# Kernel tuning notes

Measured on AMD Instinct MI355X. Metric: run time of the kernel, lower is better.

The kernel has to match this reference:

```python
import jax, jax.numpy as jnp
import numpy as np

N_NODES = 100000
N_EDGES = 3200000
NFEAT, HID, NCLASS = 256, 32, 16


def setup_inputs() -> dict:
    key = jax.random.key(0)
    ks = jax.random.split(key, 6)
    x = jax.random.normal(ks[0], (N_NODES, NFEAT), dtype=jnp.float32)
    edge_index = jax.random.randint(ks[1], (2, N_EDGES), 0, N_NODES, dtype=jnp.int64)
    edge_weight = jax.random.uniform(ks[2], (N_EDGES,), dtype=jnp.float32)
    # Glorot-ish init for the two GCNConv linear weights; bias zeros (PyG default init zeros bias)
    W1 = jax.random.normal(ks[3], (NFEAT, HID), dtype=jnp.float32) * (1.0 / np.sqrt(NFEAT))
    b1 = jnp.zeros((HID,), dtype=jnp.float32)
    W2 = jax.random.normal(ks[4], (HID, NCLASS), dtype=jnp.float32) * (1.0 / np.sqrt(HID))
    b2 = jnp.zeros((NCLASS,), dtype=jnp.float32)
    return {"x": x, "edge_index": edge_index, "edge_weight": edge_weight,
            "W1": W1, "b1": b1, "W2": W2, "b2": b2}


def _gcn_norm(row, col, w, n):
    """PyG gcn_norm: add self-loops (weight 1), symmetric normalization."""
    loop = jnp.arange(n, dtype=row.dtype)
    row = jnp.concatenate([row, loop])
    col = jnp.concatenate([col, loop])
    w = jnp.concatenate([w, jnp.ones((n,), dtype=w.dtype)])
    deg = jax.ops.segment_sum(w, col, num_segments=n)  # degree at target nodes
    dinv = jnp.where(deg > 0, jax.lax.rsqrt(deg), 0.0)
    norm = dinv[row] * w * dinv[col]
    return row, col, norm


def _gcn_conv(x, W, b, row, col, norm, n):
    xw = x @ W                                  # [N, out]
    msg = xw[row] * norm[:, None]               # gather at source + scale
    out = jax.ops.segment_sum(msg, col, num_segments=n)  # scatter-add at target
    return out + b


def reference(x, edge_index, edge_weight, W1, b1, W2, b2):
    n = x.shape[0]
    row, col, norm = _gcn_norm(edge_index[0], edge_index[1], edge_weight, n)
    h = jax.nn.relu(_gcn_conv(x, W1, b1, row, col, norm, n))
    # dropout is identity in eval mode
    logits = _gcn_conv(h, W2, b2, row, col, norm, n)
    return jax.nn.log_softmax(logits, axis=1)
```

## Files before the change

### kernel.cpp

```cpp
#include <hip/hip_runtime.h>

#define N_NODES 100000
#define N_EDGES 3200000
#define NFEAT 256
#define HID 32
#define NCLASS 16

#define NB 32
#define CHUNK (N_EDGES / NB)
#define RN2 32768
#define NR2 ((N_NODES + RN2 - 1) / RN2)

#define SCAN_TPB 256
#define SCAN_EPB 1024
#define SCAN_NBLK ((N_NODES + SCAN_EPB - 1) / SCAN_EPB)

#define XPAD 261

__device__ inline unsigned short f2bf(float f) {
    unsigned u = __float_as_uint(f);
    u += 0x7FFFu + ((u >> 16) & 1u);
    return (unsigned short)(u >> 16);
}
__device__ inline float bf2f(unsigned short s) {
    return __uint_as_float((unsigned)s << 16);
}

__global__ __launch_bounds__(1024) void k_count(const int* __restrict__ col,
                                                unsigned* __restrict__ H) {
    __shared__ unsigned hist[RN2 / 2];
    int t = threadIdx.x, b = blockIdx.x, r = blockIdx.y;
    int base = r * RN2;
    const int* cc = col + (size_t)b * CHUNK;
    for (int i = t; i < RN2 / 2; i += 1024) hist[i] = 0;
    __syncthreads();
    for (int i = t; i < CHUNK; i += 1024) {
        unsigned d = (unsigned)cc[i] - (unsigned)base;
        if (d < RN2) atomicAdd(&hist[d >> 1], 1u << ((d & 1) * 16));
    }
    __syncthreads();
    int lim = min(RN2, N_NODES - base);
    unsigned* Hb = H + (size_t)b * N_NODES;
    for (int i = t; i < lim; i += 1024)
        Hb[base + i] = (hist[i >> 1] >> ((i & 1) * 16)) & 0xFFFFu;
}

__global__ void k_rowsum(const unsigned* __restrict__ H, int* __restrict__ cnt) {
    int n = blockIdx.x * 256 + threadIdx.x;
    if (n >= N_NODES) return;
    unsigned s = 0;
    #pragma unroll 8
    for (int b = 0; b < NB; ++b) s += H[(size_t)b * N_NODES + n];
    cnt[n] = (int)s;
}

__global__ __launch_bounds__(SCAN_TPB) void k_scanA(const int* __restrict__ cnt,
                                                    int* __restrict__ offs,
                                                    int* __restrict__ bsum) {
    __shared__ int s[SCAN_TPB];
    int t = threadIdx.x;
    int base = blockIdx.x * SCAN_EPB + t * 4;
    int v0 = (base + 0 < N_NODES) ? cnt[base + 0] : 0;
    int v1 = (base + 1 < N_NODES) ? cnt[base + 1] : 0;
    int v2 = (base + 2 < N_NODES) ? cnt[base + 2] : 0;
    int v3 = (base + 3 < N_NODES) ? cnt[base + 3] : 0;
    int sum = v0 + v1 + v2 + v3;
    s[t] = sum;
    __syncthreads();
    for (int off = 1; off < SCAN_TPB; off <<= 1) {
        int x = (t >= off) ? s[t - off] : 0;
        __syncthreads();
        s[t] += x;
        __syncthreads();
    }
    int excl = s[t] - sum;
    if (t == SCAN_TPB - 1) bsum[blockIdx.x] = s[t];
    int run = excl;
    if (base + 0 < N_NODES) offs[base + 0] = run; run += v0;
    if (base + 1 < N_NODES) offs[base + 1] = run; run += v1;
    if (base + 2 < N_NODES) offs[base + 2] = run; run += v2;
    if (base + 3 < N_NODES) offs[base + 3] = run;
}

__global__ __launch_bounds__(128) void k_scanB(int* __restrict__ bsum) {
    __shared__ int s[128];
    int t = threadIdx.x;
    int v = (t < SCAN_NBLK) ? bsum[t] : 0;
    s[t] = v;
    __syncthreads();
    for (int off = 1; off < 128; off <<= 1) {
        int x = (t >= off) ? s[t - off] : 0;
        __syncthreads();
        s[t] += x;
        __syncthreads();
    }
    if (t < SCAN_NBLK) bsum[t] = s[t] - v;
}

__global__ __launch_bounds__(SCAN_TPB) void k_scanC(int* __restrict__ offs,
                                                    const int* __restrict__ bsum) {
    int t = threadIdx.x;
    int add = bsum[blockIdx.x];
    int base = blockIdx.x * SCAN_EPB + t * 4;
    #pragma unroll
    for (int i = 0; i < 4; ++i) {
        int idx = base + i;
        if (idx < N_NODES) offs[idx] += add;
    }
    if (blockIdx.x == 0 && t == 0) offs[N_NODES] = N_EDGES;
}

__global__ void k_bprefix(unsigned* __restrict__ H, const int* __restrict__ offs) {
    int n = blockIdx.x * 256 + threadIdx.x;
    if (n >= N_NODES) return;
    unsigned run = (unsigned)offs[n];
    for (int b = 0; b < NB; ++b) {
        size_t idx = (size_t)b * N_NODES + n;
        unsigned v = H[idx];
        H[idx] = run;
        run += v;
    }
}

__global__ __launch_bounds__(1024) void k_place(const int* __restrict__ col,
                                                const unsigned* __restrict__ B,
                                                unsigned* __restrict__ perm) {
    __shared__ unsigned rk[RN2 / 2];
    int t = threadIdx.x, b = blockIdx.x, r = blockIdx.y;
    int base = r * RN2;
    size_t eb = (size_t)b * CHUNK;
    const unsigned* Bb = B + (size_t)b * N_NODES;
    for (int i = t; i < RN2 / 2; i += 1024) rk[i] = 0;
    __syncthreads();
    for (int i = t; i < CHUNK; i += 1024) {
        int c = col[eb + i];
        unsigned d = (unsigned)c - (unsigned)base;
        if (d < RN2) {
            unsigned old = atomicAdd(&rk[d >> 1], 1u << ((d & 1) * 16));
            unsigned rr = (old >> ((d & 1) * 16)) & 0xFFFFu;
            perm[eb + i] = Bb[c] + rr;
        }
    }
}

__global__ void k_emit(const int* __restrict__ row, const float* __restrict__ w,
                       const unsigned* __restrict__ perm, float2* __restrict__ ein) {
    int e = blockIdx.x * 256 + threadIdx.x;
    if (e < N_EDGES) ein[perm[e]] = make_float2(__int_as_float(row[e]), w[e]);
}

__global__ void k_deg(const float2* __restrict__ ein, const int* __restrict__ offs,
                      float* __restrict__ dinv) {
    int idx = blockIdx.x * 256 + threadIdx.x;
    int n = idx >> 2, l = idx & 3;
    if (n >= N_NODES) return;
    int s = offs[n], e = offs[n + 1];
    float sum = 0.f;
    for (int p = s + l; p < e; p += 4) sum += ein[p].y;
    sum += __shfl_xor(sum, 1, 4);
    sum += __shfl_xor(sum, 2, 4);
    if (l == 0) dinv[n] = rsqrtf(1.0f + sum);
}

__global__ void k_norm(float2* __restrict__ ein, const int* __restrict__ offs,
                       const float* __restrict__ dinv) {
    int idx = blockIdx.x * 256 + threadIdx.x;
    int n = idx >> 2, l = idx & 3;
    if (n >= N_NODES) return;
    float dn = dinv[n];
    int s = offs[n], e = offs[n + 1];
    for (int p = s + l; p < e; p += 4) {
        float2 v = ein[p];
        int src = __float_as_int(v.x);
        ein[p].y = dn * dinv[src] * v.y;
    }
}

__global__ __launch_bounds__(256) void k_gemm1s(const float* __restrict__ x,
                                                const float* __restrict__ W1,
                                                unsigned short* __restrict__ xwp) {
    __shared__ float sWc[16 * HID];
    __shared__ float sX[16 * XPAD];
    int t = threadIdx.x;
    long rowbase = (long)blockIdx.x * 256;
    int kbase = blockIdx.y * 64;
    unsigned short* xw = xwp + (size_t)blockIdx.y * N_NODES * HID;
    int tr = t >> 3;
    int tc = t & 7;
    float acc[8][4] = {};
    for (int k0 = kbase; k0 < kbase + 64; k0 += 16) {
        if (t < 128) *(float4*)&sWc[t * 4] = *(const float4*)&W1[k0 * HID + t * 4];
        #pragma unroll
        for (int p = 0; p < 4; ++p) {
            int rt = (t >> 2) + p * 64;
            int kk = (t & 3) * 4;
            long grow = rowbase + rt;
            float4 v = make_float4(0.f, 0.f, 0.f, 0.f);
            if (grow < N_NODES) v = *(const float4*)&x[grow * NFEAT + k0 + kk];
            sX[(kk + 0) * XPAD + rt] = v.x; sX[(kk + 1) * XPAD + rt] = v.y;
            sX[(kk + 2) * XPAD + rt] = v.z; sX[(kk + 3) * XPAD + rt] = v.w;
        }
        __syncthreads();
        #pragma unroll
        for (int kk = 0; kk < 16; ++kk) {
            float xv[8], wv[4];
            *(float4*)&xv[0] = *(float4*)&sX[kk * XPAD + tr * 8];
            *(float4*)&xv[4] = *(float4*)&sX[kk * XPAD + tr * 8 + 4];
            *(float4*)&wv[0] = *(float4*)&sWc[kk * HID + tc * 4];
            #pragma unroll
            for (int m = 0; m < 8; ++m)
                #pragma unroll
                for (int n = 0; n < 4; ++n)
                    acc[m][n] = fmaf(xv[m], wv[n], acc[m][n]);
        }
        __syncthreads();
    }
    #pragma unroll
    for (int m = 0; m < 8; ++m) {
        long r = rowbase + tr * 8 + m;
        if (r < N_NODES) {
            ushort4 o;
            o.x = f2bf(acc[m][0]); o.y = f2bf(acc[m][1]);
            o.z = f2bf(acc[m][2]); o.w = f2bf(acc[m][3]);
            *(ushort4*)&xw[r * HID + tc * 4] = o;
        }
    }
}

__global__ void k_comb(const unsigned short* __restrict__ xwp,
                       ushort4* __restrict__ xwb) {
    int i = blockIdx.x * 256 + threadIdx.x;
    const ushort4* p0 = (const ushort4*)xwp;
    const ushort4* p1 = p0 + 800000;
    const ushort4* p2 = p1 + 800000;
    const ushort4* p3 = p2 + 800000;
    ushort4 a = p0[i], b = p1[i], c = p2[i], d = p3[i];
    ushort4 o;
    o.x = f2bf(bf2f(a.x) + bf2f(b.x) + bf2f(c.x) + bf2f(d.x));
    o.y = f2bf(bf2f(a.y) + bf2f(b.y) + bf2f(c.y) + bf2f(d.y));
    o.z = f2bf(bf2f(a.z) + bf2f(b.z) + bf2f(c.z) + bf2f(d.z));
    o.w = f2bf(bf2f(a.w) + bf2f(b.w) + bf2f(c.w) + bf2f(d.w));
    xwb[i] = o;
}

__global__ __launch_bounds__(256) void k_gather1(const unsigned short* __restrict__ xwb,
                                                 const float* __restrict__ dinv,
                                                 const float2* __restrict__ ein,
                                                 const int* __restrict__ offs,
                                                 const float* __restrict__ b1,
                                                 float* __restrict__ h) {
    int idx = blockIdx.x * 256 + threadIdx.x;
    int n = idx >> 3, l = idx & 7;
    int c4 = l * 4;
    const ushort4* xb = (const ushort4*)xwb;
    float di = dinv[n];
    float dd = di * di;
    ushort4 q = xb[(long)n * 8 + l];
    float4 acc = make_float4(bf2f(q.x) * dd, bf2f(q.y) * dd,
                             bf2f(q.z) * dd, bf2f(q.w) * dd);
    int s = offs[n], e = offs[n + 1];
    for (int p0 = s; p0 < e; p0 += 8) {
        int pl = p0 + l;
        float2 pr = (pl < e) ? ein[pl] : make_float2(__int_as_float(n), 0.f);
        int ri = __float_as_int(pr.x);
        #pragma unroll
        for (int j = 0; j < 8; ++j) {
            int r = __shfl(ri, j, 8);
            float nm = __shfl(pr.y, j, 8);
            ushort4 g = xb[(long)r * 8 + l];
            acc.x = fmaf(bf2f(g.x), nm, acc.x);
            acc.y = fmaf(bf2f(g.y), nm, acc.y);
            acc.z = fmaf(bf2f(g.z), nm, acc.z);
            acc.w = fmaf(bf2f(g.w), nm, acc.w);
        }
    }
    float4 bb = *(const float4*)&b1[c4];
    acc.x = fmaxf(acc.x + bb.x, 0.f);
    acc.y = fmaxf(acc.y + bb.y, 0.f);
    acc.z = fmaxf(acc.z + bb.z, 0.f);
    acc.w = fmaxf(acc.w + bb.w, 0.f);
    *(float4*)&h[(long)n * HID + c4] = acc;
}

__global__ __launch_bounds__(256) void k_gemm2(const float* __restrict__ h,
                                               const float* __restrict__ W2,
                                               unsigned short* __restrict__ hwb) {
    __shared__ float sH[64][33];
    __shared__ float sW2[HID * NCLASS];
    int t = threadIdx.x;
    if (t < 128) {
        int idx = t * 4;
        *(float4*)&sW2[idx] = *(const float4*)&W2[idx];
    }
    long base = (long)blockIdx.x * 64;
    #pragma unroll
    for (int i = 0; i < 2; ++i) {
        int idx = t + i * 256;
        int rt = idx >> 3, kk = (idx & 7) * 4;
        long gr = base + rt;
        float4 v = make_float4(0.f, 0.f, 0.f, 0.f);
        if (gr < N_NODES) v = *(const float4*)&h[gr * HID + kk];
        sH[rt][kk + 0] = v.x; sH[rt][kk + 1] = v.y;
        sH[rt][kk + 2] = v.z; sH[rt][kk + 3] = v.w;
    }
    __syncthreads();
    int r = t >> 2, c4 = (t & 3) * 4;
    float acc[4] = {};
    #pragma unroll
    for (int k = 0; k < HID; ++k) {
        float hv = sH[r][k];
        float wv[4];
        *(float4*)&wv[0] = *(float4*)&sW2[k * NCLASS + c4];
        #pragma unroll
        for (int n = 0; n < 4; ++n) acc[n] = fmaf(hv, wv[n], acc[n]);
    }
    long gr = base + r;
    if (gr < N_NODES) {
        ushort4 o;
        o.x = f2bf(acc[0]); o.y = f2bf(acc[1]);
        o.z = f2bf(acc[2]); o.w = f2bf(acc[3]);
        *(ushort4*)&hwb[gr * NCLASS + c4] = o;
    }
}

__global__ __launch_bounds__(256) void k_gather2(const unsigned short* __restrict__ hwb,
                                                 const float* __restrict__ dinv,
                                                 const float2* __restrict__ ein,
                                                 const int* __restrict__ offs,
                                                 const float* __restrict__ b2,
                                                 float* __restrict__ out) {
    int idx = blockIdx.x * 256 + threadIdx.x;
    int n = idx >> 2, l = idx & 3;
    if (n >= N_NODES) return;
    int c4 = l * 4;
    const ushort4* hb = (const ushort4*)hwb;
    float di = dinv[n];
    float dd = di * di;
    ushort4 q = hb[(long)n * 4 + l];
    float4 acc = make_float4(bf2f(q.x) * dd, bf2f(q.y) * dd,
                             bf2f(q.z) * dd, bf2f(q.w) * dd);
    int s = offs[n], e = offs[n + 1];
    for (int p0 = s; p0 < e; p0 += 8) {
        int pl0 = p0 + l, pl1 = p0 + 4 + l;
        float2 pr0 = (pl0 < e) ? ein[pl0] : make_float2(__int_as_float(n), 0.f);
        float2 pr1 = (pl1 < e) ? ein[pl1] : make_float2(__int_as_float(n), 0.f);
        int r0 = __float_as_int(pr0.x), r1 = __float_as_int(pr1.x);
        #pragma unroll
        for (int j = 0; j < 4; ++j) {
            int r = __shfl(r0, j, 4);
            float nm = __shfl(pr0.y, j, 4);
            ushort4 g = hb[(long)r * 4 + l];
            acc.x = fmaf(bf2f(g.x), nm, acc.x);
            acc.y = fmaf(bf2f(g.y), nm, acc.y);
            acc.z = fmaf(bf2f(g.z), nm, acc.z);
            acc.w = fmaf(bf2f(g.w), nm, acc.w);
        }
        #pragma unroll
        for (int j = 0; j < 4; ++j) {
            int r = __shfl(r1, j, 4);
            float nm = __shfl(pr1.y, j, 4);
            ushort4 g = hb[(long)r * 4 + l];
            acc.x = fmaf(bf2f(g.x), nm, acc.x);
            acc.y = fmaf(bf2f(g.y), nm, acc.y);
            acc.z = fmaf(bf2f(g.z), nm, acc.z);
            acc.w = fmaf(bf2f(g.w), nm, acc.w);
        }
    }
    float4 bb = *(const float4*)&b2[c4];
    float vx = acc.x + bb.x, vy = acc.y + bb.y, vz = acc.z + bb.z, vw = acc.w + bb.w;
    float m = fmaxf(fmaxf(vx, vy), fmaxf(vz, vw));
    m = fmaxf(m, __shfl_xor(m, 1, 4));
    m = fmaxf(m, __shfl_xor(m, 2, 4));
    float sum = __expf(vx - m) + __expf(vy - m) + __expf(vz - m) + __expf(vw - m);
    sum += __shfl_xor(sum, 1, 4);
    sum += __shfl_xor(sum, 2, 4);
    float ls = m + __logf(sum);
    float4 o = make_float4(vx - ls, vy - ls, vz - ls, vw - ls);
    *(float4*)&out[(long)n * NCLASS + c4] = o;
}

extern "C" void kernel_launch(void* const* d_in, const int* in_sizes, int n_in,
                              void* d_out, int out_size, void* d_ws, size_t ws_size,
                              hipStream_t stream) {
    const float* x  = (const float*)d_in[0];
    const int*   ei = (const int*)d_in[1];
    const float* w  = (const float*)d_in[2];
    const float* W1 = (const float*)d_in[3];
    const float* b1 = (const float*)d_in[4];
    const float* W2 = (const float*)d_in[5];
    const float* b2 = (const float*)d_in[6];
    float* out = (float*)d_out;

    const int* row = ei;
    const int* col = ei + N_EDGES;

    float* ws = (float*)d_ws;
    float2* ein = (float2*)ws;
    unsigned* H = (unsigned*)(ws + 2 * (size_t)N_EDGES);
    unsigned* perm = (unsigned*)(ws + 2 * (size_t)N_EDGES + (size_t)NB * N_NODES);
    float* h = (float*)perm;
    float* dinv = ws + 2 * (size_t)N_EDGES + (size_t)NB * N_NODES + N_EDGES;
    int* cnt = (int*)(dinv + N_NODES);
    int* offs = cnt + N_NODES;
    int* bsum = offs + N_NODES + 1;
    size_t xwp_off = (size_t)(2 * (size_t)N_EDGES + (size_t)NB * N_NODES + N_EDGES
                              + 3 * N_NODES + 1 + 128);
    xwp_off = (xwp_off + 3) & ~(size_t)3;
    unsigned short* xwp = (unsigned short*)(ws + xwp_off);
    unsigned short* xwb = (unsigned short*)(ws + xwp_off + 6400000);
    unsigned short* hwb = xwb + (size_t)N_NODES * HID;

    const int B = 256;

    k_count<<<dim3(NB, NR2), 1024, 0, stream>>>(col, H);
    k_rowsum<<<(N_NODES + B - 1) / B, B, 0, stream>>>(H, cnt);
    k_scanA<<<SCAN_NBLK, SCAN_TPB, 0, stream>>>(cnt, offs, bsum);
    k_scanB<<<1, 128, 0, stream>>>(bsum);
    k_scanC<<<SCAN_NBLK, SCAN_TPB, 0, stream>>>(offs, bsum);
    k_bprefix<<<(N_NODES + B - 1) / B, B, 0, stream>>>(H, offs);
    k_place<<<dim3(NB, NR2), 1024, 0, stream>>>(col, H, perm);
    k_emit<<<(N_EDGES + B - 1) / B, B, 0, stream>>>(row, w, perm, ein);

    k_deg<<<(N_NODES * 4 + B - 1) / B, B, 0, stream>>>(ein, offs, dinv);
    k_norm<<<(N_NODES * 4 + B - 1) / B, B, 0, stream>>>(ein, offs, dinv);

    k_gemm1s<<<dim3((N_NODES + 255) / 256, 4), 256, 0, stream>>>(x, W1, xwp);
    k_comb<<<(N_NODES * HID / 4) / B, B, 0, stream>>>(xwp, (ushort4*)xwb);
    k_gather1<<<(N_NODES * 8) / B, B, 0, stream>>>(xwb, dinv, ein, offs, b1, h);

    k_gemm2<<<(N_NODES + 63) / 64, B, 0, stream>>>(h, W2, hwb);
    k_gather2<<<(N_NODES * 4 + B - 1) / B, B, 0, stream>>>(hwb, dinv, ein, offs, b2, out);
}
```

Measured before the change: 312.2 us.

## Fold edge normalization into gathers and retile first GEMM split-K

Removes the separate k_norm pass that rewrote every edge weight with dinv[src]*dinv[dst]. Instead the gathers scale each edge weight by dinv[src] at load time and apply the destination dinv once at the end. This avoids a full read-modify-write sweep over the 3.2M-edge array, at the price of an extra random dinv lookup per edge in both gathers. Separately, the first GEMM now uses 128-row tiles with 2-way split-K over 128 features instead of 256-row tiles with 4-way split-K. That halves the partial-result traffic that k_comb has to combine, but gives each thread less register blocking.

```diff
diff --git a/kernel.cpp b/kernel.cpp
--- a/kernel.cpp
+++ b/kernel.cpp
@@ -15,7 +15,7 @@
 #define SCAN_EPB 1024
 #define SCAN_NBLK ((N_NODES + SCAN_EPB - 1) / SCAN_EPB)
 
-#define XPAD 261
+#define XPAD 133
 
 __device__ inline unsigned short f2bf(float f) {
     unsigned u = __float_as_uint(f);
@@ -162,38 +162,24 @@
     if (l == 0) dinv[n] = rsqrtf(1.0f + sum);
 }
 
-__global__ void k_norm(float2* __restrict__ ein, const int* __restrict__ offs,
-                       const float* __restrict__ dinv) {
-    int idx = blockIdx.x * 256 + threadIdx.x;
-    int n = idx >> 2, l = idx & 3;
-    if (n >= N_NODES) return;
-    float dn = dinv[n];
-    int s = offs[n], e = offs[n + 1];
-    for (int p = s + l; p < e; p += 4) {
-        float2 v = ein[p];
-        int src = __float_as_int(v.x);
-        ein[p].y = dn * dinv[src] * v.y;
-    }
-}
-
 __global__ __launch_bounds__(256) void k_gemm1s(const float* __restrict__ x,
                                                 const float* __restrict__ W1,
                                                 unsigned short* __restrict__ xwp) {
-    __shared__ float sWc[16 * HID];
-    __shared__ float sX[16 * XPAD];
+    __shared__ float sWc[32 * HID];
+    __shared__ float sX[32 * XPAD];
     int t = threadIdx.x;
-    long rowbase = (long)blockIdx.x * 256;
-    int kbase = blockIdx.y * 64;
+    long rowbase = (long)blockIdx.x * 128;
+    int kbase = blockIdx.y * 128;
     unsigned short* xw = xwp + (size_t)blockIdx.y * N_NODES * HID;
     int tr = t >> 3;
     int tc = t & 7;
-    float acc[8][4] = {};
-    for (int k0 = kbase; k0 < kbase + 64; k0 += 16) {
-        if (t < 128) *(float4*)&sWc[t * 4] = *(const float4*)&W1[k0 * HID + t * 4];
+    float acc[4][4] = {};
+    for (int k0 = kbase; k0 < kbase + 128; k0 += 32) {
+        *(float4*)&sWc[t * 4] = *(const float4*)&W1[k0 * HID + t * 4];
         #pragma unroll
         for (int p = 0; p < 4; ++p) {
-            int rt = (t >> 2) + p * 64;
-            int kk = (t & 3) * 4;
+            int rt = (t >> 3) + p * 32;
+            int kk = (t & 7) * 4;
             long grow = rowbase + rt;
             float4 v = make_float4(0.f, 0.f, 0.f, 0.f);
             if (grow < N_NODES) v = *(const float4*)&x[grow * NFEAT + k0 + kk];
@@ -201,14 +187,16 @@
             sX[(kk + 2) * XPAD + rt] = v.z; sX[(kk + 3) * XPAD + rt] = v.w;
         }
         __syncthreads();
-        #pragma unroll
-        for (int kk = 0; kk < 16; ++kk) {
-            float xv[8], wv[4];
-            *(float4*)&xv[0] = *(float4*)&sX[kk * XPAD + tr * 8];
-            *(float4*)&xv[4] = *(float4*)&sX[kk * XPAD + tr * 8 + 4];
+        #pragma unroll 8
+        for (int kk = 0; kk < 32; ++kk) {
+            float xv[4], wv[4];
+            xv[0] = sX[kk * XPAD + tr * 4 + 0];
+            xv[1] = sX[kk * XPAD + tr * 4 + 1];
+            xv[2] = sX[kk * XPAD + tr * 4 + 2];
+            xv[3] = sX[kk * XPAD + tr * 4 + 3];
             *(float4*)&wv[0] = *(float4*)&sWc[kk * HID + tc * 4];
             #pragma unroll
-            for (int m = 0; m < 8; ++m)
+            for (int m = 0; m < 4; ++m)
                 #pragma unroll
                 for (int n = 0; n < 4; ++n)
                     acc[m][n] = fmaf(xv[m], wv[n], acc[m][n]);
@@ -216,8 +204,8 @@
         __syncthreads();
     }
     #pragma unroll
-    for (int m = 0; m < 8; ++m) {
-        long r = rowbase + tr * 8 + m;
+    for (int m = 0; m < 4; ++m) {
+        long r = rowbase + tr * 4 + m;
         if (r < N_NODES) {
             ushort4 o;
             o.x = f2bf(acc[m][0]); o.y = f2bf(acc[m][1]);
@@ -232,14 +220,12 @@
     int i = blockIdx.x * 256 + threadIdx.x;
     const ushort4* p0 = (const ushort4*)xwp;
     const ushort4* p1 = p0 + 800000;
-    const ushort4* p2 = p1 + 800000;
-    const ushort4* p3 = p2 + 800000;
-    ushort4 a = p0[i], b = p1[i], c = p2[i], d = p3[i];
+    ushort4 a = p0[i], b = p1[i];
     ushort4 o;
-    o.x = f2bf(bf2f(a.x) + bf2f(b.x) + bf2f(c.x) + bf2f(d.x));
-    o.y = f2bf(bf2f(a.y) + bf2f(b.y) + bf2f(c.y) + bf2f(d.y));
-    o.z = f2bf(bf2f(a.z) + bf2f(b.z) + bf2f(c.z) + bf2f(d.z));
-    o.w = f2bf(bf2f(a.w) + bf2f(b.w) + bf2f(c.w) + bf2f(d.w));
+    o.x = f2bf(bf2f(a.x) + bf2f(b.x));
+    o.y = f2bf(bf2f(a.y) + bf2f(b.y));
+    o.z = f2bf(bf2f(a.z) + bf2f(b.z));
+    o.w = f2bf(bf2f(a.w) + bf2f(b.w));
     xwb[i] = o;
 }
 
@@ -254,15 +240,15 @@
     int c4 = l * 4;
     const ushort4* xb = (const ushort4*)xwb;
     float di = dinv[n];
-    float dd = di * di;
     ushort4 q = xb[(long)n * 8 + l];
-    float4 acc = make_float4(bf2f(q.x) * dd, bf2f(q.y) * dd,
-                             bf2f(q.z) * dd, bf2f(q.w) * dd);
+    float4 acc = make_float4(bf2f(q.x) * di, bf2f(q.y) * di,
+                             bf2f(q.z) * di, bf2f(q.w) * di);
     int s = offs[n], e = offs[n + 1];
     for (int p0 = s; p0 < e; p0 += 8) {
         int pl = p0 + l;
         float2 pr = (pl < e) ? ein[pl] : make_float2(__int_as_float(n), 0.f);
         int ri = __float_as_int(pr.x);
+        pr.y *= dinv[ri];
         #pragma unroll
         for (int j = 0; j < 8; ++j) {
             int r = __shfl(ri, j, 8);
@@ -275,10 +261,10 @@
         }
     }
     float4 bb = *(const float4*)&b1[c4];
-    acc.x = fmaxf(acc.x + bb.x, 0.f);
-    acc.y = fmaxf(acc.y + bb.y, 0.f);
-    acc.z = fmaxf(acc.z + bb.z, 0.f);
-    acc.w = fmaxf(acc.w + bb.w, 0.f);
+    acc.x = fmaxf(fmaf(acc.x, di, bb.x), 0.f);
+    acc.y = fmaxf(fmaf(acc.y, di, bb.y), 0.f);
+    acc.z = fmaxf(fmaf(acc.z, di, bb.z), 0.f);
+    acc.w = fmaxf(fmaf(acc.w, di, bb.w), 0.f);
     *(float4*)&h[(long)n * HID + c4] = acc;
 }
 
@@ -335,16 +321,17 @@
     int c4 = l * 4;
     const ushort4* hb = (const ushort4*)hwb;
     float di = dinv[n];
-    float dd = di * di;
     ushort4 q = hb[(long)n * 4 + l];
-    float4 acc = make_float4(bf2f(q.x) * dd, bf2f(q.y) * dd,
-                             bf2f(q.z) * dd, bf2f(q.w) * dd);
+    float4 acc = make_float4(bf2f(q.x) * di, bf2f(q.y) * di,
+                             bf2f(q.z) * di, bf2f(q.w) * di);
     int s = offs[n], e = offs[n + 1];
     for (int p0 = s; p0 < e; p0 += 8) {
         int pl0 = p0 + l, pl1 = p0 + 4 + l;
         float2 pr0 = (pl0 < e) ? ein[pl0] : make_float2(__int_as_float(n), 0.f);
         float2 pr1 = (pl1 < e) ? ein[pl1] : make_float2(__int_as_float(n), 0.f);
         int r0 = __float_as_int(pr0.x), r1 = __float_as_int(pr1.x);
+        pr0.y *= dinv[r0];
+        pr1.y *= dinv[r1];
         #pragma unroll
         for (int j = 0; j < 4; ++j) {
             int r = __shfl(r0, j, 4);
@@ -367,7 +354,8 @@
         }
     }
     float4 bb = *(const float4*)&b2[c4];
-    float vx = acc.x + bb.x, vy = acc.y + bb.y, vz = acc.z + bb.z, vw = acc.w + bb.w;
+    float vx = fmaf(acc.x, di, bb.x), vy = fmaf(acc.y, di, bb.y);
+    float vz = fmaf(acc.z, di, bb.z), vw = fmaf(acc.w, di, bb.w);
     float m = fmaxf(fmaxf(vx, vy), fmaxf(vz, vw));
     m = fmaxf(m, __shfl_xor(m, 1, 4));
     m = fmaxf(m, __shfl_xor(m, 2, 4));
@@ -407,7 +395,7 @@
                               + 3 * N_NODES + 1 + 128);
     xwp_off = (xwp_off + 3) & ~(size_t)3;
     unsigned short* xwp = (unsigned short*)(ws + xwp_off);
-    unsigned short* xwb = (unsigned short*)(ws + xwp_off + 6400000);
+    unsigned short* xwb = (unsigned short*)(ws + xwp_off + 3200000);
     unsigned short* hwb = xwb + (size_t)N_NODES * HID;
 
     const int B = 256;
@@ -422,9 +410,8 @@
     k_emit<<<(N_EDGES + B - 1) / B, B, 0, stream>>>(row, w, perm, ein);
 
     k_deg<<<(N_NODES * 4 + B - 1) / B, B, 0, stream>>>(ein, offs, dinv);
-    k_norm<<<(N_NODES * 4 + B - 1) / B, B, 0, stream>>>(ein, offs, dinv);
-
-    k_gemm1s<<<dim3((N_NODES + 255) / 256, 4), 256, 0, stream>>>(x, W1, xwp);
+
+    k_gemm1s<<<dim3((N_NODES + 127) / 128, 2), 256, 0, stream>>>(x, W1, xwp);
     k_comb<<<(N_NODES * HID / 4) / B, B, 0, stream>>>(xwp, (ushort4*)xwb);
     k_gather1<<<(N_NODES * 8) / B, B, 0, stream>>>(xwb, dinv, ein, offs, b1, h);
 
```

After: 307.8 us. No clear change (-1.4%).
